# Kernel optimization log

Hardware: AMD Instinct MI355X
Metric: run time of the kernel (lower is better)

## Reference

```python
import jax, jax.numpy as jnp
import numpy as np

B, N, DIM = 4, 2048, 512
HEADS, DK = 8, 64
SCALE = DK ** -0.5


def setup_inputs() -> dict:
    key = jax.random.key(0)
    k1, k2, k3, k4 = jax.random.split(key, 4)
    x = jax.random.normal(k1, (B, N, DIM), dtype=jnp.float32)
    # nn.Linear(dim, dim_key*heads, bias=False): y = x @ W.T; store W already transposed
    Wq = jax.random.normal(k2, (DIM, HEADS * DK), dtype=jnp.float32) * (DIM ** -0.5)
    Wk = jax.random.normal(k3, (DIM, HEADS * DK), dtype=jnp.float32) * (DIM ** -0.5)
    rel_content_bias = jax.random.normal(k4, (1, HEADS, 1, DK), dtype=jnp.float32)
    return {"x": x, "Wq": Wq, "Wk": Wk, "rel_content_bias": rel_content_bias}


def _split_heads(t, h):
    # [b, n, h*d] -> [b, h, n, d]
    b, n, hd = t.shape
    return t.reshape(b, n, h, hd // h).transpose(0, 2, 1, 3)


def reference(x, Wq, Wk, rel_content_bias):
    q = _split_heads(x @ Wq, HEADS) * SCALE          # [b, h, n, dk]
    k = _split_heads(x @ Wk, HEADS)                  # [b, h, n, dk]
    v = _split_heads(x, HEADS)                       # [b, h, n, dim/h]
    logits = jnp.einsum('bhid,bhjd->bhij', q + rel_content_bias, k)
    attn = jax.nn.sigmoid(logits)                    # no softmax normalization
    out = jnp.einsum('bhij,bhjd->bhid', attn, v)     # [b, h, n, dim/h]
    b, h, n, d = out.shape
    return out.transpose(0, 2, 1, 3).reshape(b, n, h * d)
```

## Files before the change

### kernel.cpp

```cpp
#include <hip/hip_runtime.h>
#include <hip/hip_bf16.h>
#include <stdint.h>

#define BB 4
#define NN 2048
#define DIMD 512
#define HH 8
#define DKK 64
#define MTOT (BB * NN)
constexpr float SCALE = 0.125f;

typedef __attribute__((ext_vector_type(4))) float f32x4;
typedef __attribute__((ext_vector_type(2))) float f32x2;
typedef __attribute__((ext_vector_type(8))) short bf16x8;
typedef __attribute__((ext_vector_type(4))) _Float16 f16x4;
typedef __attribute__((ext_vector_type(2))) __fp16 fp16v2;
typedef __attribute__((ext_vector_type(4))) __fp16 fp16v4;
typedef __attribute__((ext_vector_type(2))) unsigned int u32x2;

union pack8 { unsigned short s[8]; uint4 v; };
union fragu { u32x2 h[2]; bf16x8 v; };

__device__ __forceinline__ unsigned short f2bf(float f) {
  union { float f; uint32_t u; } v; v.f = f;
  uint32_t u = v.u;
  return (unsigned short)((u + 0x7FFFu + ((u >> 16) & 1u)) >> 16);
}

__device__ __forceinline__ unsigned short f2h(float f) {
  union { _Float16 h; unsigned short u; } c; c.h = (_Float16)f;
  return c.u;
}

__device__ __forceinline__ bf16x8 ld_frag(const unsigned short* p) {
  fragu f;
  f.h[0] = *(const u32x2*)p;
  f.h[1] = *(const u32x2*)(p + 4);
  return f.v;
}
__device__ __forceinline__ void st8(unsigned short* p, uint4 v) {
  *(u32x2*)p = (u32x2){v.x, v.y};
  *(u32x2*)(p + 4) = (u32x2){v.z, v.w};
}

__device__ __forceinline__ f16x4 sig_pack(f32x4 sv) {
  float e0 = __expf(-__builtin_fabsf(sv[0]));
  float e1 = __expf(-__builtin_fabsf(sv[1]));
  float e2 = __expf(-__builtin_fabsf(sv[2]));
  float e3 = __expf(-__builtin_fabsf(sv[3]));
  const f32x2 c3 = {-0.22184f, -0.22184f};
  const f32x2 c2 = {0.66550f, 0.66550f};
  const f32x2 c1 = {-0.94280f, -0.94280f};
  const f32x2 c0 = {0.49826f, 0.49826f};
  f32x2 eA = {e0, e1}, eB = {e2, e3};
  f32x2 pA = __builtin_elementwise_fma(
      __builtin_elementwise_fma(__builtin_elementwise_fma(c3, eA, c2), eA, c1),
      eA, c0);
  f32x2 pB = __builtin_elementwise_fma(
      __builtin_elementwise_fma(__builtin_elementwise_fma(c3, eB, c2), eB, c1),
      eB, c0);
  float r0 = __builtin_copysignf(pA.x, sv[0]) + 0.5f;
  float r1 = __builtin_copysignf(pA.y, sv[1]) + 0.5f;
  float r2 = __builtin_copysignf(pB.x, sv[2]) + 0.5f;
  float r3 = __builtin_copysignf(pB.y, sv[3]) + 0.5f;
  fp16v2 lo = __builtin_amdgcn_cvt_pkrtz(r0, r1);
  fp16v2 hi = __builtin_amdgcn_cvt_pkrtz(r2, r3);
  fp16v4 p;
  p.x = lo.x; p.y = lo.y; p.z = hi.x; p.w = hi.y;
  return __builtin_bit_cast(f16x4, p);
}

__global__ __launch_bounds__(256) void prep(const float* __restrict__ x,
                                            const float* __restrict__ wq,
                                            const float* __restrict__ wk,
                                            unsigned short* __restrict__ xb,
                                            unsigned short* __restrict__ xtf,
                                            unsigned short* __restrict__ wtq,
                                            unsigned short* __restrict__ wtk) {
  const int bx = blockIdx.x, tid = threadIdx.x;
  if (bx < 2048) {
    size_t base = ((size_t)bx * 256 + tid) * 8;
    float4 a = *(const float4*)(x + base);
    float4 b = *(const float4*)(x + base + 4);
    pack8 p;
    p.s[0] = f2bf(a.x); p.s[1] = f2bf(a.y); p.s[2] = f2bf(a.z); p.s[3] = f2bf(a.w);
    p.s[4] = f2bf(b.x); p.s[5] = f2bf(b.y); p.s[6] = f2bf(b.z); p.s[7] = f2bf(b.w);
    *(uint4*)(xb + base) = p.v;
  } else if (bx < 2304) {
    int q = bx - 2048;
    int b = q >> 6, r = q & 63;
    int dt = r >> 3, nt = r & 7;
    int d = dt * 64 + (tid & 63);
    int n0 = nt * 256 + (tid >> 6) * 64;
    const float* xp = x + ((size_t)b * NN + n0) * DIMD + d;
    unsigned short* dp = xtf + ((size_t)b * DIMD + d) * NN + n0;
#pragma unroll
    for (int g = 0; g < 8; g++) {
      pack8 pa;
#pragma unroll
      for (int k = 0; k < 8; k++) pa.s[k] = f2h(xp[(size_t)(g * 8 + k) * DIMD]);
      *(uint4*)(dp + g * 8) = pa.v;
    }
  } else {
    __shared__ __align__(16) unsigned short T[64][68];
    int q = bx - 2304;
    const float* w = (q >= 64) ? wk : wq;
    unsigned short* wt = (q >= 64) ? wtk : wtq;
    int r = q & 63;
    int kt = r >> 3, nt = r & 7;
    const int k0 = kt * 64, n0 = nt * 64;
#pragma unroll
    for (int rr = 0; rr < 16; rr++) {
      int idx = tid + rr * 256;
      int kl = idx >> 6, nl = idx & 63;
      T[nl][kl] = f2bf(w[(size_t)(k0 + kl) * DIMD + n0 + nl]);
    }
    __syncthreads();
#pragma unroll
    for (int rr = 0; rr < 2; rr++) {
      int idx = tid + rr * 256;
      int nl = idx >> 3, c = idx & 7;
      fragu f;
      f.h[0] = *(const u32x2*)&T[nl][c * 8];
      f.h[1] = *(const u32x2*)&T[nl][c * 8 + 4];
      uint4 v;
      v.x = f.h[0].x; v.y = f.h[0].y; v.z = f.h[1].x; v.w = f.h[1].y;
      *(uint4*)(wt + (size_t)(n0 + nl) * DIMD + k0 + c * 8) = v;
    }
  }
}

__global__ __launch_bounds__(512) void qk_gemm(const unsigned short* __restrict__ xb,
                                               const unsigned short* __restrict__ wtq,
                                               const unsigned short* __restrict__ wtk,
                                               const float* __restrict__ bias,
                                               unsigned short* __restrict__ qout,
                                               unsigned short* __restrict__ kout) {
  __shared__ __align__(16) unsigned short Als[128][68];
  __shared__ __align__(16) unsigned short Bls[128][68];
  const int mb = blockIdx.x, nb = blockIdx.y;
  const bool isQ = (nb < 4);
  const unsigned short* wt = isQ ? wtq : wtk;
  unsigned short* outp = isQ ? qout : kout;
  const int n0 = (nb & 3) * 128, m0 = mb * 128;
  const int tid = threadIdx.x;
  const int wave = tid >> 6, lane = tid & 63;
  const int quad = lane >> 4, l16 = lane & 15;
  const int wm = wave >> 2, wn = wave & 3;

  f32x4 acc[4][2];
#pragma unroll
  for (int a = 0; a < 4; a++)
#pragma unroll
    for (int c = 0; c < 2; c++) acc[a][c] = (f32x4){0.f, 0.f, 0.f, 0.f};

  for (int k0 = 0; k0 < DIMD; k0 += 64) {
    __syncthreads();
#pragma unroll
    for (int r = 0; r < 2; r++) {
      int idx = tid + r * 512;
      int row = idx >> 3, c = idx & 7;
      st8(&Als[row][c * 8], *(const uint4*)(xb + (size_t)(m0 + row) * DIMD + k0 + c * 8));
      st8(&Bls[row][c * 8], *(const uint4*)(wt + (size_t)(n0 + row) * DIMD + k0 + c * 8));
    }
    __syncthreads();
#pragma unroll
    for (int ks = 0; ks < 2; ks++) {
      bf16x8 af[4], bfr[2];
#pragma unroll
      for (int t = 0; t < 4; t++)
        af[t] = ld_frag(&Als[wm * 64 + t * 16 + l16][quad * 8 + ks * 32]);
#pragma unroll
      for (int t = 0; t < 2; t++)
        bfr[t] = ld_frag(&Bls[wn * 32 + t * 16 + l16][quad * 8 + ks * 32]);
#pragma unroll
      for (int tm = 0; tm < 4; tm++)
#pragma unroll
        for (int tn = 0; tn < 2; tn++)
          acc[tm][tn] =
              __builtin_amdgcn_mfma_f32_16x16x32_bf16(af[tm], bfr[tn], acc[tm][tn], 0, 0, 0);
    }
  }
#pragma unroll
  for (int tm = 0; tm < 4; tm++) {
#pragma unroll
    for (int tn = 0; tn < 2; tn++) {
#pragma unroll
      for (int r = 0; r < 4; r++) {
        int row = m0 + wm * 64 + tm * 16 + quad * 4 + r;
        int gcol = n0 + wn * 32 + tn * 16 + l16;
        float v = acc[tm][tn][r];
        if (isQ) v = v * SCALE + bias[gcol];
        outp[(size_t)row * DIMD + gcol] = f2bf(v);
      }
    }
  }
}

__global__ __launch_bounds__(1024) void attn(const unsigned short* __restrict__ qb,
                                             const unsigned short* __restrict__ kb,
                                             const unsigned short* __restrict__ xtf,
                                             float* __restrict__ out) {
  __shared__ __align__(16) char smem[69632];
  unsigned short* Kall = (unsigned short*)smem;
  unsigned short* Vall = Kall + 4 * 64 * 68;
  float* R0 = (float*)smem;
  float* R1 = R0 + 128 * 66;

  const int it = blockIdx.x, bh = blockIdx.y;
  const int b = bh >> 3, h = bh & 7;
  const int i0 = it * 128;
  const int tid = threadIdx.x;
  const int lane = tid & 63;
  const int grp = tid >> 8;
  const int wv = (tid >> 6) & 3;
  const int gtid = tid & 255;
  const int quad = lane >> 4, l16 = lane & 15;

  bf16x8 qf[2][2];
  int irow[2];
#pragma unroll
  for (int s_ = 0; s_ < 2; s_++) {
    irow[s_] = i0 + wv * 32 + s_ * 16 + l16;
    const unsigned short* qp = qb + ((size_t)b * NN + irow[s_]) * DIMD + h * DKK + quad * 8;
    qf[s_][0] = *(const bf16x8*)qp;
    qf[s_][1] = *(const bf16x8*)(qp + 32);
  }

  f32x4 o[2][4];
#pragma unroll
  for (int s_ = 0; s_ < 2; s_++)
#pragma unroll
    for (int td = 0; td < 4; td++) o[s_][td] = (f32x4){0.f, 0.f, 0.f, 0.f};

  const unsigned short* kbase = kb + (size_t)b * NN * DIMD + h * DKK;
  const unsigned short* vbase = xtf + ((size_t)b * DIMD + h * DKK) * NN;
  unsigned short* Kg = Kall + grp * (64 * 68);
  unsigned short* Vg = Vall + grp * (64 * 68);
  const int jbase = grp * 512;

  for (int itr = 0; itr < 8; itr++) {
    const int j0 = jbase + itr * 64;
    __syncthreads();
#pragma unroll
    for (int r = 0; r < 2; r++) {
      int idx = gtid + r * 256;
      int row = idx >> 3, c = idx & 7;
      st8(&Kg[row * 68 + c * 8], *(const uint4*)(kbase + (size_t)(j0 + row) * DIMD + c * 8));
      st8(&Vg[row * 68 + c * 8], *(const uint4*)(vbase + (size_t)row * NN + j0 + c * 8));
    }
    __syncthreads();

#pragma unroll
    for (int t = 0; t < 4; t++) {
      bf16x8 kf0 = ld_frag(&Kg[(t * 16 + l16) * 68 + quad * 8]);
      bf16x8 kf1 = ld_frag(&Kg[(t * 16 + l16) * 68 + quad * 8 + 32]);
      f16x4 pf[2];
#pragma unroll
      for (int s_ = 0; s_ < 2; s_++) {
        f32x4 sv = (f32x4){0.f, 0.f, 0.f, 0.f};
        sv = __builtin_amdgcn_mfma_f32_16x16x32_bf16(kf0, qf[s_][0], sv, 0, 0, 0);
        sv = __builtin_amdgcn_mfma_f32_16x16x32_bf16(kf1, qf[s_][1], sv, 0, 0, 0);
        pf[s_] = sig_pack(sv);
      }
#pragma unroll
      for (int td = 0; td < 4; td++) {
        f16x4 vf = __builtin_bit_cast(
            f16x4, *(const u32x2*)&Vg[(td * 16 + l16) * 68 + t * 16 + quad * 4]);
        o[0][td] = __builtin_amdgcn_mfma_f32_16x16x16f16(vf, pf[0], o[0][td], 0, 0, 0);
        o[1][td] = __builtin_amdgcn_mfma_f32_16x16x16f16(vf, pf[1], o[1][td], 0, 0, 0);
      }
    }
  }

  __syncthreads();
  if (grp == 1 || grp == 3) {
    float* R = (grp == 1) ? R0 : R1;
#pragma unroll
    for (int s_ = 0; s_ < 2; s_++)
#pragma unroll
      for (int td = 0; td < 4; td++) {
        int base = (wv * 32 + s_ * 16 + l16) * 66 + td * 16 + quad * 4;
        *(f32x2*)&R[base] = (f32x2){o[s_][td][0], o[s_][td][1]};
        *(f32x2*)&R[base + 2] = (f32x2){o[s_][td][2], o[s_][td][3]};
      }
  }
  __syncthreads();
  if (grp == 0 || grp == 2) {
    float* R = (grp == 0) ? R0 : R1;
#pragma unroll
    for (int s_ = 0; s_ < 2; s_++)
#pragma unroll
      for (int td = 0; td < 4; td++) {
        int base = (wv * 32 + s_ * 16 + l16) * 66 + td * 16 + quad * 4;
        f32x2 a = *(const f32x2*)&R[base];
        f32x2 c = *(const f32x2*)&R[base + 2];
        o[s_][td][0] += a.x; o[s_][td][1] += a.y;
        o[s_][td][2] += c.x; o[s_][td][3] += c.y;
      }
  }
  __syncthreads();
  if (grp == 2) {
#pragma unroll
    for (int s_ = 0; s_ < 2; s_++)
#pragma unroll
      for (int td = 0; td < 4; td++) {
        int base = (wv * 32 + s_ * 16 + l16) * 66 + td * 16 + quad * 4;
        *(f32x2*)&R0[base] = (f32x2){o[s_][td][0], o[s_][td][1]};
        *(f32x2*)&R0[base + 2] = (f32x2){o[s_][td][2], o[s_][td][3]};
      }
  }
  __syncthreads();
  if (grp == 0) {
#pragma unroll
    for (int s_ = 0; s_ < 2; s_++) {
#pragma unroll
      for (int td = 0; td < 4; td++) {
        int base = (wv * 32 + s_ * 16 + l16) * 66 + td * 16 + quad * 4;
        f32x2 a = *(const f32x2*)&R0[base];
        f32x2 c = *(const f32x2*)&R0[base + 2];
        o[s_][td][0] += a.x; o[s_][td][1] += a.y;
        o[s_][td][2] += c.x; o[s_][td][3] += c.y;
        float* op = out + ((size_t)b * NN + irow[s_]) * DIMD + h * DKK + td * 16 + quad * 4;
        *(f32x4*)op = o[s_][td];
      }
    }
  }
}

extern "C" void kernel_launch(void* const* d_in, const int* in_sizes, int n_in,
                              void* d_out, int out_size, void* d_ws, size_t ws_size,
                              hipStream_t stream) {
  const float* x = (const float*)d_in[0];
  const float* Wq = (const float*)d_in[1];
  const float* Wk = (const float*)d_in[2];
  const float* bias = (const float*)d_in[3];
  float* out = (float*)d_out;

  unsigned short* ws = (unsigned short*)d_ws;
  unsigned short* xb = ws;
  unsigned short* xtf = xb + (size_t)MTOT * DIMD;
  unsigned short* wtq = xtf + (size_t)MTOT * DIMD;
  unsigned short* wtk = wtq + (size_t)DIMD * DIMD;
  unsigned short* qb = wtk + (size_t)DIMD * DIMD;
  unsigned short* kb = qb + (size_t)MTOT * DIMD;

  prep<<<dim3(2432), 256, 0, stream>>>(x, Wq, Wk, xb, xtf, wtq, wtk);
  qk_gemm<<<dim3(64, 8), 512, 0, stream>>>(xb, wtq, wtk, bias, qb, kb);
  attn<<<dim3(16, 32), 1024, 0, stream>>>(qb, kb, xtf, out);
}
```

Baseline: 175.4 us.

## Prefetch next tiles into registers and halve attention block to two key groups

Both the QK GEMM and the attention kernel now load the next K-step tile into registers before computing on the current one, so global load latency overlaps the MFMA work. The attention kernel drops from four key-split groups of 256 threads to two groups of 512 threads total. Each group covers 1024 keys, which halves the LDS footprint and simplifies the cross-group reduction to a single exchange. Launch bounds now request 4 blocks per CU, which could limit registers and cause spills, and there is less intra-block parallelism per query tile.

```diff
diff --git a/kernel.cpp b/kernel.cpp
--- a/kernel.cpp
+++ b/kernel.cpp
@@ -130,12 +130,12 @@
   }
 }
 
-__global__ __launch_bounds__(512) void qk_gemm(const unsigned short* __restrict__ xb,
-                                               const unsigned short* __restrict__ wtq,
-                                               const unsigned short* __restrict__ wtk,
-                                               const float* __restrict__ bias,
-                                               unsigned short* __restrict__ qout,
-                                               unsigned short* __restrict__ kout) {
+__global__ __launch_bounds__(512, 4) void qk_gemm(const unsigned short* __restrict__ xb,
+                                                  const unsigned short* __restrict__ wtq,
+                                                  const unsigned short* __restrict__ wtk,
+                                                  const float* __restrict__ bias,
+                                                  unsigned short* __restrict__ qout,
+                                                  unsigned short* __restrict__ kout) {
   __shared__ __align__(16) unsigned short Als[128][68];
   __shared__ __align__(16) unsigned short Bls[128][68];
   const int mb = blockIdx.x, nb = blockIdx.y;
@@ -154,16 +154,30 @@
 #pragma unroll
     for (int c = 0; c < 2; c++) acc[a][c] = (f32x4){0.f, 0.f, 0.f, 0.f};
 
+  const int srow[2] = {tid >> 3, (tid + 512) >> 3};
+  const int scol = (tid & 7) * 8;
+  uint4 pa[2], pb[2];
+#pragma unroll
+  for (int r = 0; r < 2; r++) {
+    pa[r] = *(const uint4*)(xb + (size_t)(m0 + srow[r]) * DIMD + scol);
+    pb[r] = *(const uint4*)(wt + (size_t)(n0 + srow[r]) * DIMD + scol);
+  }
+
   for (int k0 = 0; k0 < DIMD; k0 += 64) {
     __syncthreads();
 #pragma unroll
     for (int r = 0; r < 2; r++) {
-      int idx = tid + r * 512;
-      int row = idx >> 3, c = idx & 7;
-      st8(&Als[row][c * 8], *(const uint4*)(xb + (size_t)(m0 + row) * DIMD + k0 + c * 8));
-      st8(&Bls[row][c * 8], *(const uint4*)(wt + (size_t)(n0 + row) * DIMD + k0 + c * 8));
-    }
-    __syncthreads();
+      st8(&Als[srow[r]][scol], pa[r]);
+      st8(&Bls[srow[r]][scol], pb[r]);
+    }
+    __syncthreads();
+    if (k0 + 64 < DIMD) {
+#pragma unroll
+      for (int r = 0; r < 2; r++) {
+        pa[r] = *(const uint4*)(xb + (size_t)(m0 + srow[r]) * DIMD + k0 + 64 + scol);
+        pb[r] = *(const uint4*)(wt + (size_t)(n0 + srow[r]) * DIMD + k0 + 64 + scol);
+      }
+    }
 #pragma unroll
     for (int ks = 0; ks < 2; ks++) {
       bf16x8 af[4], bfr[2];
@@ -197,15 +211,14 @@
   }
 }
 
-__global__ __launch_bounds__(1024) void attn(const unsigned short* __restrict__ qb,
-                                             const unsigned short* __restrict__ kb,
-                                             const unsigned short* __restrict__ xtf,
-                                             float* __restrict__ out) {
-  __shared__ __align__(16) char smem[69632];
+__global__ __launch_bounds__(512, 4) void attn(const unsigned short* __restrict__ qb,
+                                               const unsigned short* __restrict__ kb,
+                                               const unsigned short* __restrict__ xtf,
+                                               float* __restrict__ out) {
+  __shared__ __align__(16) char smem[34816];
   unsigned short* Kall = (unsigned short*)smem;
-  unsigned short* Vall = Kall + 4 * 64 * 68;
+  unsigned short* Vall = Kall + 2 * 64 * 68;
   float* R0 = (float*)smem;
-  float* R1 = R0 + 128 * 66;
 
   const int it = blockIdx.x, bh = blockIdx.y;
   const int b = bh >> 3, h = bh & 7;
@@ -237,19 +250,33 @@
   const unsigned short* vbase = xtf + ((size_t)b * DIMD + h * DKK) * NN;
   unsigned short* Kg = Kall + grp * (64 * 68);
   unsigned short* Vg = Vall + grp * (64 * 68);
-  const int jbase = grp * 512;
-
-  for (int itr = 0; itr < 8; itr++) {
-    const int j0 = jbase + itr * 64;
+  const int jbase = grp * 1024;
+
+  const int trow[2] = {gtid >> 3, (gtid + 256) >> 3};
+  const int tcol = (gtid & 7) * 8;
+  uint4 pk[2], pv[2];
+#pragma unroll
+  for (int r = 0; r < 2; r++) {
+    pk[r] = *(const uint4*)(kbase + (size_t)(jbase + trow[r]) * DIMD + tcol);
+    pv[r] = *(const uint4*)(vbase + (size_t)trow[r] * NN + jbase + tcol);
+  }
+
+  for (int itr = 0; itr < 16; itr++) {
     __syncthreads();
 #pragma unroll
     for (int r = 0; r < 2; r++) {
-      int idx = gtid + r * 256;
-      int row = idx >> 3, c = idx & 7;
-      st8(&Kg[row * 68 + c * 8], *(const uint4*)(kbase + (size_t)(j0 + row) * DIMD + c * 8));
-      st8(&Vg[row * 68 + c * 8], *(const uint4*)(vbase + (size_t)row * NN + j0 + c * 8));
-    }
-    __syncthreads();
+      st8(&Kg[trow[r] * 68 + tcol], pk[r]);
+      st8(&Vg[trow[r] * 68 + tcol], pv[r]);
+    }
+    __syncthreads();
+    if (itr < 15) {
+      const int j0 = jbase + (itr + 1) * 64;
+#pragma unroll
+      for (int r = 0; r < 2; r++) {
+        pk[r] = *(const uint4*)(kbase + (size_t)(j0 + trow[r]) * DIMD + tcol);
+        pv[r] = *(const uint4*)(vbase + (size_t)trow[r] * NN + j0 + tcol);
+      }
+    }
 
 #pragma unroll
     for (int t = 0; t < 4; t++) {
@@ -274,33 +301,7 @@
   }
 
   __syncthreads();
-  if (grp == 1 || grp == 3) {
-    float* R = (grp == 1) ? R0 : R1;
-#pragma unroll
-    for (int s_ = 0; s_ < 2; s_++)
-#pragma unroll
-      for (int td = 0; td < 4; td++) {
-        int base = (wv * 32 + s_ * 16 + l16) * 66 + td * 16 + quad * 4;
-        *(f32x2*)&R[base] = (f32x2){o[s_][td][0], o[s_][td][1]};
-        *(f32x2*)&R[base + 2] = (f32x2){o[s_][td][2], o[s_][td][3]};
-      }
-  }
-  __syncthreads();
-  if (grp == 0 || grp == 2) {
-    float* R = (grp == 0) ? R0 : R1;
-#pragma unroll
-    for (int s_ = 0; s_ < 2; s_++)
-#pragma unroll
-      for (int td = 0; td < 4; td++) {
-        int base = (wv * 32 + s_ * 16 + l16) * 66 + td * 16 + quad * 4;
-        f32x2 a = *(const f32x2*)&R[base];
-        f32x2 c = *(const f32x2*)&R[base + 2];
-        o[s_][td][0] += a.x; o[s_][td][1] += a.y;
-        o[s_][td][2] += c.x; o[s_][td][3] += c.y;
-      }
-  }
-  __syncthreads();
-  if (grp == 2) {
+  if (grp == 1) {
 #pragma unroll
     for (int s_ = 0; s_ < 2; s_++)
 #pragma unroll
@@ -347,5 +348,5 @@
 
   prep<<<dim3(2432), 256, 0, stream>>>(x, Wq, Wk, xb, xtf, wtq, wtk);
   qk_gemm<<<dim3(64, 8), 512, 0, stream>>>(xb, wtq, wtk, bias, qb, kb);
-  attn<<<dim3(16, 32), 1024, 0, stream>>>(qb, kb, xtf, out);
-}
+  attn<<<dim3(16, 32), 512, 0, stream>>>(qb, kb, xtf, out);
+}
```

Result: faster. 158.4 us (-9.7%).
